# Optimization experiments

Hardware: AMD Instinct MI355X
Metric: run time of the kernel (lower is better)

Reference implementation:

```python
import jax, jax.numpy as jnp
import numpy as np

NUM_LEVELS = 8
BASE_RES = 16
MAX_RES = 1024
TABLE_SIZE = 2 ** 17
FEAT = 2
ALPHA_SHIFT = 5.0
ALPHA_SCALE = 1.0

_growth = np.exp((np.log(MAX_RES) - np.log(BASE_RES)) / (NUM_LEVELS - 1))
SCALINGS = np.floor(BASE_RES * _growth ** np.arange(NUM_LEVELS)).astype(np.float32)  # per-level grid res
CORNERS = np.array([[(i >> 2) & 1, (i >> 1) & 1, i & 1] for i in range(8)], dtype=np.int32)  # voxel corners
PRIMES = np.array([1, 2654435761, 805459861], dtype=np.uint32)  # nerfstudio hash primes


def hash_encode(pos, table):
    # pos: [N,3] in [0,1]; table: [NUM_LEVELS*TABLE_SIZE, FEAT]
    scaled = pos[:, None, :] * jnp.asarray(SCALINGS)[None, :, None]              # [N,L,3]
    f = jnp.floor(scaled)
    w = scaled - f                                                               # trilinear weights
    idx = f.astype(jnp.int32)[:, :, None, :] + jnp.asarray(CORNERS)[None, None]  # [N,L,8,3]
    h = idx.astype(jnp.uint32) * jnp.asarray(PRIMES)
    hashed = (h[..., 0] ^ h[..., 1] ^ h[..., 2]) % TABLE_SIZE                    # [N,L,8]
    hashed = hashed.astype(jnp.int32) + (jnp.arange(NUM_LEVELS, dtype=jnp.int32) * TABLE_SIZE)[None, :, None]
    feats = table[hashed]                                                        # [N,L,8,F] gather
    cw = jnp.where(jnp.asarray(CORNERS)[None, None] == 1, w[:, :, None, :], 1.0 - w[:, :, None, :]).prod(-1)
    out = (feats * cw[..., None]).sum(2)                                         # [N,L,F]
    return out.reshape(pos.shape[0], NUM_LEVELS * FEAT)


def setup_inputs():
    key = jax.random.key(0)
    ks = jax.random.split(key, 8)
    R, S = 8192, 48
    return {
        "positions": jax.random.normal(ks[0], (R, S, 3), jnp.float32),
        "c2ws": jax.random.normal(ks[1], (R, 3, 4), jnp.float32) * 0.5,
        "aabb": jnp.array([[-1.0, -1.0, -1.0], [1.0, 1.0, 1.0]], jnp.float32),
        "table": jax.random.uniform(ks[2], (NUM_LEVELS * TABLE_SIZE, FEAT), jnp.float32, -1e-4, 1e-4),
        "w1": jax.random.normal(ks[3], (16, 32), jnp.float32) * 0.25,
        "b1": jnp.zeros((32,), jnp.float32),
        "w2": jax.random.normal(ks[4], (32, 16), jnp.float32) * 0.18,
        "b2": jnp.zeros((16,), jnp.float32),
        "hw1": jax.random.normal(ks[5], (16, 64), jnp.float32) * 0.25,
        "hb1": jnp.zeros((64,), jnp.float32),
        "hw2": jax.random.normal(ks[6], (64, 1), jnp.float32) * 0.125,
        "hb2": jnp.zeros((1,), jnp.float32),
    }


def reference(positions, c2ws, aabb, table, w1, b1, w2, b2, hw1, hb1, hw2, hb2):
    R, S = positions.shape[:2]
    rot = c2ws[:, :3, :3]
    trans = c2ws[:, :3, 3]
    rot_t = jnp.swapaxes(rot, 1, 2)                          # w2c rotation = R^T
    t_w2c = -jnp.einsum('rij,rj->ri', rot_t, trans)          # w2c translation = -R^T t
    pos = jnp.einsum('rij,rsj->rsi', rot_t, positions) + t_w2c[:, None, :]
    pos = (pos - aabb[0]) / (aabb[1] - aabb[0])              # SceneBox.get_normalized_positions
    selector = jnp.all((pos > 0.0) & (pos < 1.0), axis=-1)   # inside unit cube
    pos = pos * selector[..., None]
    enc = hash_encode(pos.reshape(-1, 3), table)             # [N, 16]
    h = jax.nn.relu(enc @ w1 + b1) @ w2 + b2                 # mlp_base -> geo features
    o = jax.nn.relu(h @ hw1 + hb1) @ hw2 + hb2               # mlp_head -> alpha logits
    o = o.reshape(R, S, -1)
    return ALPHA_SCALE * jax.nn.sigmoid(o - ALPHA_SHIFT) * selector[..., None]
```

## Files before the change

kernel.cpp:

```cpp
#include <hip/hip_runtime.h>
#include <math.h>
#include <stdint.h>

#define NLEV 8
#define TSIZE 131072
#define TMASK (TSIZE - 1)

__global__ __launch_bounds__(256, 4) void rif_kernel(
    const float* __restrict__ positions,
    const float* __restrict__ c2ws,
    const float* __restrict__ aabb,
    const float* __restrict__ table,
    const float* __restrict__ w1, const float* __restrict__ b1,
    const float* __restrict__ w2, const float* __restrict__ b2,
    const float* __restrict__ hw1, const float* __restrict__ hb1,
    const float* __restrict__ hw2, const float* __restrict__ hb2,
    float* __restrict__ out, int total, int S)
{
    __shared__ float sw1[512];
    __shared__ float sb1[32];
    __shared__ float sw2[512];
    __shared__ float sb2[16];
    __shared__ float shw1[1024];
    __shared__ float shb1[64];
    __shared__ float shw2[64];
    __shared__ float shb2[1];

    for (int i = threadIdx.x; i < 512; i += 256) { sw1[i] = w1[i]; sw2[i] = w2[i]; }
    for (int i = threadIdx.x; i < 1024; i += 256) shw1[i] = hw1[i];
    if (threadIdx.x < 64) { shb1[threadIdx.x] = hb1[threadIdx.x]; shw2[threadIdx.x] = hw2[threadIdx.x]; }
    if (threadIdx.x < 32) sb1[threadIdx.x] = b1[threadIdx.x];
    if (threadIdx.x < 16) sb2[threadIdx.x] = b2[threadIdx.x];
    if (threadIdx.x == 0) shb2[0] = hb2[0];
    __syncthreads();

    int gid = blockIdx.x * blockDim.x + threadIdx.x;
    if (gid >= total) return;
    int r = gid / S;

    const float* p = positions + (size_t)gid * 3;
    const float* c = c2ws + (size_t)r * 12;
    float px = p[0], py = p[1], pz = p[2];
    float c00 = c[0], c01 = c[1], c02 = c[2],  t0 = c[3];
    float c10 = c[4], c11 = c[5], c12 = c[6],  t1 = c[7];
    float c20 = c[8], c21 = c[9], c22 = c[10], t2 = c[11];

    float m0 = __fadd_rn(__fadd_rn(__fmul_rn(c00, px), __fmul_rn(c10, py)), __fmul_rn(c20, pz));
    float m1 = __fadd_rn(__fadd_rn(__fmul_rn(c01, px), __fmul_rn(c11, py)), __fmul_rn(c21, pz));
    float m2 = __fadd_rn(__fadd_rn(__fmul_rn(c02, px), __fmul_rn(c12, py)), __fmul_rn(c22, pz));
    float n0 = __fadd_rn(__fadd_rn(__fmul_rn(c00, t0), __fmul_rn(c10, t1)), __fmul_rn(c20, t2));
    float n1 = __fadd_rn(__fadd_rn(__fmul_rn(c01, t0), __fmul_rn(c11, t1)), __fmul_rn(c21, t2));
    float n2 = __fadd_rn(__fadd_rn(__fmul_rn(c02, t0), __fmul_rn(c12, t1)), __fmul_rn(c22, t2));
    float posx = __fsub_rn(m0, n0);
    float posy = __fsub_rn(m1, n1);
    float posz = __fsub_rn(m2, n2);

    float a0x = aabb[0], a0y = aabb[1], a0z = aabb[2];
    float a1x = aabb[3], a1y = aabb[4], a1z = aabb[5];
    posx = __fdiv_rn(__fsub_rn(posx, a0x), __fsub_rn(a1x, a0x));
    posy = __fdiv_rn(__fsub_rn(posy, a0y), __fsub_rn(a1y, a0y));
    posz = __fdiv_rn(__fsub_rn(posz, a0z), __fsub_rn(a1z, a0z));

    bool sel = (posx > 0.f) & (posx < 1.f) & (posy > 0.f) & (posy < 1.f) & (posz > 0.f) & (posz < 1.f);
    if (!sel) { out[gid] = 0.f; return; }

    const float kScale[8] = {16.f, 28.f, 52.f, 95.f, 172.f, 312.f, 565.f, 1024.f};

    float wxs[8], wys[8], wzs[8];
    float2 ft[8][8];
    #pragma unroll
    for (int l = 0; l < NLEV; ++l) {
        float sc = kScale[l];
        float sx = posx * sc, sy = posy * sc, sz = posz * sc;
        float fx = floorf(sx), fy = floorf(sy), fz = floorf(sz);
        wxs[l] = sx - fx; wys[l] = sy - fy; wzs[l] = sz - fz;
        uint32_t ix = (uint32_t)(int)fx, iy = (uint32_t)(int)fy, iz = (uint32_t)(int)fz;
        uint32_t hy0 = iy * 2654435761u, hy1 = hy0 + 2654435761u;
        uint32_t hz0 = iz * 805459861u,  hz1 = hz0 + 805459861u;
        const float2* tab = (const float2*)table + (size_t)l * TSIZE;
        #pragma unroll
        for (int cc = 0; cc < 8; ++cc) {
            uint32_t cx = (cc >> 2) & 1, cy = (cc >> 1) & 1, cz = cc & 1;
            uint32_t hh = ((ix + cx) ^ (cy ? hy1 : hy0) ^ (cz ? hz1 : hz0)) & TMASK;
            ft[l][cc] = tab[hh];
        }
    }

    float enc[16];
    #pragma unroll
    for (int l = 0; l < NLEV; ++l) {
        float wx = wxs[l], wy = wys[l], wz = wzs[l];
        float ux = 1.f - wx, uy = 1.f - wy, uz = 1.f - wz;
        float q00 = uy * uz, q01 = uy * wz, q10 = wy * uz, q11 = wy * wz;
        float f0, f1;
        f0 = ft[l][0].x * (ux * q00); f1 = ft[l][0].y * (ux * q00);
        f0 = fmaf(ft[l][1].x, ux * q01, f0); f1 = fmaf(ft[l][1].y, ux * q01, f1);
        f0 = fmaf(ft[l][2].x, ux * q10, f0); f1 = fmaf(ft[l][2].y, ux * q10, f1);
        f0 = fmaf(ft[l][3].x, ux * q11, f0); f1 = fmaf(ft[l][3].y, ux * q11, f1);
        f0 = fmaf(ft[l][4].x, wx * q00, f0); f1 = fmaf(ft[l][4].y, wx * q00, f1);
        f0 = fmaf(ft[l][5].x, wx * q01, f0); f1 = fmaf(ft[l][5].y, wx * q01, f1);
        f0 = fmaf(ft[l][6].x, wx * q10, f0); f1 = fmaf(ft[l][6].y, wx * q10, f1);
        f0 = fmaf(ft[l][7].x, wx * q11, f0); f1 = fmaf(ft[l][7].y, wx * q11, f1);
        enc[2 * l] = f0;
        enc[2 * l + 1] = f1;
    }

    float h1[32];
    #pragma unroll
    for (int j = 0; j < 32; ++j) h1[j] = sb1[j];
    #pragma unroll
    for (int i = 0; i < 16; ++i) {
        float e = enc[i];
        #pragma unroll
        for (int j = 0; j < 32; ++j) h1[j] = fmaf(e, sw1[i * 32 + j], h1[j]);
    }
    #pragma unroll
    for (int j = 0; j < 32; ++j) h1[j] = fmaxf(h1[j], 0.f);

    float h2[16];
    #pragma unroll
    for (int j = 0; j < 16; ++j) h2[j] = sb2[j];
    #pragma unroll
    for (int i = 0; i < 32; ++i) {
        float e = h1[i];
        #pragma unroll
        for (int j = 0; j < 16; ++j) h2[j] = fmaf(e, sw2[i * 16 + j], h2[j]);
    }

    float o = shb2[0];
    #pragma unroll
    for (int j = 0; j < 64; ++j) {
        float acc = shb1[j];
        #pragma unroll
        for (int i = 0; i < 16; ++i) acc = fmaf(h2[i], shw1[i * 64 + j], acc);
        o = fmaf(fmaxf(acc, 0.f), shw2[j], o);
    }

    float x = o - 5.0f;
    out[gid] = 1.0f / (1.0f + expf(-x));
}

extern "C" void kernel_launch(void* const* d_in, const int* in_sizes, int n_in,
                              void* d_out, int out_size, void* d_ws, size_t ws_size,
                              hipStream_t stream) {
    const float* positions = (const float*)d_in[0];
    const float* c2ws      = (const float*)d_in[1];
    const float* aabb      = (const float*)d_in[2];
    const float* table     = (const float*)d_in[3];
    const float* w1  = (const float*)d_in[4];
    const float* b1  = (const float*)d_in[5];
    const float* w2  = (const float*)d_in[6];
    const float* b2  = (const float*)d_in[7];
    const float* hw1 = (const float*)d_in[8];
    const float* hb1 = (const float*)d_in[9];
    const float* hw2 = (const float*)d_in[10];
    const float* hb2 = (const float*)d_in[11];

    int R = in_sizes[1] / 12;
    int total = in_sizes[0] / 3;
    int S = total / R;

    int threads = 256;
    int blocks = (total + threads - 1) / threads;
    hipLaunchKernelGGL(rif_kernel, dim3(blocks), dim3(threads), 0, stream,
                       positions, c2ws, aabb, table,
                       w1, b1, w2, b2, hw1, hb1, hw2, hb2,
                       (float*)d_out, total, S);
}
```

Before: 69.09 us.

## Compact in-box samples via atomic index list before hash encoding and MLP

Measured after the change: 140.0 us. +102.6%, slower.

```diff
diff --git a/kernel.cpp b/kernel.cpp
--- a/kernel.cpp
+++ b/kernel.cpp
@@ -6,7 +6,95 @@
 #define TSIZE 131072
 #define TMASK (TSIZE - 1)
 
-__global__ __launch_bounds__(256, 4) void rif_kernel(
+__device__ __forceinline__ void transform_pos(
+    const float* __restrict__ positions, const float* __restrict__ c2ws,
+    const float* __restrict__ aabb, int gid, int S,
+    float& posx, float& posy, float& posz, bool& sel)
+{
+    int r = gid / S;
+    const float* p = positions + (size_t)gid * 3;
+    const float* c = c2ws + (size_t)r * 12;
+    float px = p[0], py = p[1], pz = p[2];
+    float c00 = c[0], c01 = c[1], c02 = c[2],  t0 = c[3];
+    float c10 = c[4], c11 = c[5], c12 = c[6],  t1 = c[7];
+    float c20 = c[8], c21 = c[9], c22 = c[10], t2 = c[11];
+
+    float m0 = __fadd_rn(__fadd_rn(__fmul_rn(c00, px), __fmul_rn(c10, py)), __fmul_rn(c20, pz));
+    float m1 = __fadd_rn(__fadd_rn(__fmul_rn(c01, px), __fmul_rn(c11, py)), __fmul_rn(c21, pz));
+    float m2 = __fadd_rn(__fadd_rn(__fmul_rn(c02, px), __fmul_rn(c12, py)), __fmul_rn(c22, pz));
+    float n0 = __fadd_rn(__fadd_rn(__fmul_rn(c00, t0), __fmul_rn(c10, t1)), __fmul_rn(c20, t2));
+    float n1 = __fadd_rn(__fadd_rn(__fmul_rn(c01, t0), __fmul_rn(c11, t1)), __fmul_rn(c21, t2));
+    float n2 = __fadd_rn(__fadd_rn(__fmul_rn(c02, t0), __fmul_rn(c12, t1)), __fmul_rn(c22, t2));
+    float x0 = __fsub_rn(m0, n0);
+    float x1 = __fsub_rn(m1, n1);
+    float x2 = __fsub_rn(m2, n2);
+
+    float a0x = aabb[0], a0y = aabb[1], a0z = aabb[2];
+    float a1x = aabb[3], a1y = aabb[4], a1z = aabb[5];
+    posx = __fdiv_rn(__fsub_rn(x0, a0x), __fsub_rn(a1x, a0x));
+    posy = __fdiv_rn(__fsub_rn(x1, a0y), __fsub_rn(a1y, a0y));
+    posz = __fdiv_rn(__fsub_rn(x2, a0z), __fsub_rn(a1z, a0z));
+    sel = (posx > 0.f) & (posx < 1.f) & (posy > 0.f) & (posy < 1.f) & (posz > 0.f) & (posz < 1.f);
+}
+
+__device__ __forceinline__ float mlp_and_sigmoid(
+    const float* enc,
+    const float* sw1, const float* sb1, const float* sw2, const float* sb2,
+    const float* shw1, const float* shb1, const float* shw2, const float* shb2)
+{
+    float h1[32];
+    #pragma unroll
+    for (int j = 0; j < 32; ++j) h1[j] = sb1[j];
+    #pragma unroll
+    for (int i = 0; i < 16; ++i) {
+        float e = enc[i];
+        #pragma unroll
+        for (int j = 0; j < 32; ++j) h1[j] = fmaf(e, sw1[i * 32 + j], h1[j]);
+    }
+    #pragma unroll
+    for (int j = 0; j < 32; ++j) h1[j] = fmaxf(h1[j], 0.f);
+
+    float h2[16];
+    #pragma unroll
+    for (int j = 0; j < 16; ++j) h2[j] = sb2[j];
+    #pragma unroll
+    for (int i = 0; i < 32; ++i) {
+        float e = h1[i];
+        #pragma unroll
+        for (int j = 0; j < 16; ++j) h2[j] = fmaf(e, sw2[i * 16 + j], h2[j]);
+    }
+
+    float o = shb2[0];
+    #pragma unroll
+    for (int j = 0; j < 64; ++j) {
+        float acc = shb1[j];
+        #pragma unroll
+        for (int i = 0; i < 16; ++i) acc = fmaf(h2[i], shw1[i * 64 + j], acc);
+        o = fmaf(fmaxf(acc, 0.f), shw2[j], o);
+    }
+    float x = o - 5.0f;
+    return 1.0f / (1.0f + expf(-x));
+}
+
+__global__ __launch_bounds__(256) void rif_select(
+    const float* __restrict__ positions,
+    const float* __restrict__ c2ws,
+    const float* __restrict__ aabb,
+    float* __restrict__ out,
+    uint32_t* __restrict__ cnt,
+    uint32_t* __restrict__ idxbuf,
+    int total, int S)
+{
+    int gid = blockIdx.x * blockDim.x + threadIdx.x;
+    if (gid >= total) return;
+    float posx, posy, posz; bool sel;
+    transform_pos(positions, c2ws, aabb, gid, S, posx, posy, posz, sel);
+    if (!sel) { out[gid] = 0.f; return; }
+    uint32_t slot = atomicAdd(cnt, 1u);
+    idxbuf[slot] = (uint32_t)gid;
+}
+
+__global__ __launch_bounds__(256, 2) void rif_main(
     const float* __restrict__ positions,
     const float* __restrict__ c2ws,
     const float* __restrict__ aabb,
@@ -15,7 +103,10 @@
     const float* __restrict__ w2, const float* __restrict__ b2,
     const float* __restrict__ hw1, const float* __restrict__ hb1,
     const float* __restrict__ hw2, const float* __restrict__ hb2,
-    float* __restrict__ out, int total, int S)
+    float* __restrict__ out,
+    const uint32_t* __restrict__ cnt,
+    const uint32_t* __restrict__ idxbuf,
+    int total, int S)
 {
     __shared__ float sw1[512];
     __shared__ float sb1[32];
@@ -34,35 +125,13 @@
     if (threadIdx.x == 0) shb2[0] = hb2[0];
     __syncthreads();
 
-    int gid = blockIdx.x * blockDim.x + threadIdx.x;
-    if (gid >= total) return;
-    int r = gid / S;
-
-    const float* p = positions + (size_t)gid * 3;
-    const float* c = c2ws + (size_t)r * 12;
-    float px = p[0], py = p[1], pz = p[2];
-    float c00 = c[0], c01 = c[1], c02 = c[2],  t0 = c[3];
-    float c10 = c[4], c11 = c[5], c12 = c[6],  t1 = c[7];
-    float c20 = c[8], c21 = c[9], c22 = c[10], t2 = c[11];
-
-    float m0 = __fadd_rn(__fadd_rn(__fmul_rn(c00, px), __fmul_rn(c10, py)), __fmul_rn(c20, pz));
-    float m1 = __fadd_rn(__fadd_rn(__fmul_rn(c01, px), __fmul_rn(c11, py)), __fmul_rn(c21, pz));
-    float m2 = __fadd_rn(__fadd_rn(__fmul_rn(c02, px), __fmul_rn(c12, py)), __fmul_rn(c22, pz));
-    float n0 = __fadd_rn(__fadd_rn(__fmul_rn(c00, t0), __fmul_rn(c10, t1)), __fmul_rn(c20, t2));
-    float n1 = __fadd_rn(__fadd_rn(__fmul_rn(c01, t0), __fmul_rn(c11, t1)), __fmul_rn(c21, t2));
-    float n2 = __fadd_rn(__fadd_rn(__fmul_rn(c02, t0), __fmul_rn(c12, t1)), __fmul_rn(c22, t2));
-    float posx = __fsub_rn(m0, n0);
-    float posy = __fsub_rn(m1, n1);
-    float posz = __fsub_rn(m2, n2);
-
-    float a0x = aabb[0], a0y = aabb[1], a0z = aabb[2];
-    float a1x = aabb[3], a1y = aabb[4], a1z = aabb[5];
-    posx = __fdiv_rn(__fsub_rn(posx, a0x), __fsub_rn(a1x, a0x));
-    posy = __fdiv_rn(__fsub_rn(posy, a0y), __fsub_rn(a1y, a0y));
-    posz = __fdiv_rn(__fsub_rn(posz, a0z), __fsub_rn(a1z, a0z));
-
-    bool sel = (posx > 0.f) & (posx < 1.f) & (posy > 0.f) & (posy < 1.f) & (posz > 0.f) & (posz < 1.f);
-    if (!sel) { out[gid] = 0.f; return; }
+    uint32_t count = *cnt;
+    uint32_t i = blockIdx.x * blockDim.x + threadIdx.x;
+    if (i >= count) return;
+    int gid = (int)idxbuf[i];
+
+    float posx, posy, posz; bool sel;
+    transform_pos(positions, c2ws, aabb, gid, S, posx, posy, posz, sel);
 
     const float kScale[8] = {16.f, 28.f, 52.f, 95.f, 172.f, 312.f, 565.f, 1024.f};
 
@@ -85,6 +154,7 @@
             ft[l][cc] = tab[hh];
         }
     }
+    __builtin_amdgcn_sched_barrier(0);
 
     float enc[16];
     #pragma unroll
@@ -105,39 +175,69 @@
         enc[2 * l + 1] = f1;
     }
 
-    float h1[32];
-    #pragma unroll
-    for (int j = 0; j < 32; ++j) h1[j] = sb1[j];
-    #pragma unroll
-    for (int i = 0; i < 16; ++i) {
-        float e = enc[i];
-        #pragma unroll
-        for (int j = 0; j < 32; ++j) h1[j] = fmaf(e, sw1[i * 32 + j], h1[j]);
-    }
-    #pragma unroll
-    for (int j = 0; j < 32; ++j) h1[j] = fmaxf(h1[j], 0.f);
-
-    float h2[16];
-    #pragma unroll
-    for (int j = 0; j < 16; ++j) h2[j] = sb2[j];
-    #pragma unroll
-    for (int i = 0; i < 32; ++i) {
-        float e = h1[i];
-        #pragma unroll
-        for (int j = 0; j < 16; ++j) h2[j] = fmaf(e, sw2[i * 16 + j], h2[j]);
-    }
-
-    float o = shb2[0];
-    #pragma unroll
-    for (int j = 0; j < 64; ++j) {
-        float acc = shb1[j];
-        #pragma unroll
-        for (int i = 0; i < 16; ++i) acc = fmaf(h2[i], shw1[i * 64 + j], acc);
-        o = fmaf(fmaxf(acc, 0.f), shw2[j], o);
-    }
-
-    float x = o - 5.0f;
-    out[gid] = 1.0f / (1.0f + expf(-x));
+    out[gid] = mlp_and_sigmoid(enc, sw1, sb1, sw2, sb2, shw1, shb1, shw2, shb2);
+}
+
+__global__ __launch_bounds__(256, 4) void rif_mono(
+    const float* __restrict__ positions,
+    const float* __restrict__ c2ws,
+    const float* __restrict__ aabb,
+    const float* __restrict__ table,
+    const float* __restrict__ w1, const float* __restrict__ b1,
+    const float* __restrict__ w2, const float* __restrict__ b2,
+    const float* __restrict__ hw1, const float* __restrict__ hb1,
+    const float* __restrict__ hw2, const float* __restrict__ hb2,
+    float* __restrict__ out, int total, int S)
+{
+    __shared__ float sw1[512];
+    __shared__ float sb1[32];
+    __shared__ float sw2[512];
+    __shared__ float sb2[16];
+    __shared__ float shw1[1024];
+    __shared__ float shb1[64];
+    __shared__ float shw2[64];
+    __shared__ float shb2[1];
+
+    for (int i = threadIdx.x; i < 512; i += 256) { sw1[i] = w1[i]; sw2[i] = w2[i]; }
+    for (int i = threadIdx.x; i < 1024; i += 256) shw1[i] = hw1[i];
+    if (threadIdx.x < 64) { shb1[threadIdx.x] = hb1[threadIdx.x]; shw2[threadIdx.x] = hw2[threadIdx.x]; }
+    if (threadIdx.x < 32) sb1[threadIdx.x] = b1[threadIdx.x];
+    if (threadIdx.x < 16) sb2[threadIdx.x] = b2[threadIdx.x];
+    if (threadIdx.x == 0) shb2[0] = hb2[0];
+    __syncthreads();
+
+    int gid = blockIdx.x * blockDim.x + threadIdx.x;
+    if (gid >= total) return;
+    float posx, posy, posz; bool sel;
+    transform_pos(positions, c2ws, aabb, gid, S, posx, posy, posz, sel);
+    if (!sel) { out[gid] = 0.f; return; }
+
+    const float kScale[8] = {16.f, 28.f, 52.f, 95.f, 172.f, 312.f, 565.f, 1024.f};
+    float enc[16];
+    #pragma unroll
+    for (int l = 0; l < NLEV; ++l) {
+        float sc = kScale[l];
+        float sx = posx * sc, sy = posy * sc, sz = posz * sc;
+        float fx = floorf(sx), fy = floorf(sy), fz = floorf(sz);
+        float wx = sx - fx, wy = sy - fy, wz = sz - fz;
+        uint32_t ix = (uint32_t)(int)fx, iy = (uint32_t)(int)fy, iz = (uint32_t)(int)fz;
+        uint32_t hy0 = iy * 2654435761u, hy1 = hy0 + 2654435761u;
+        uint32_t hz0 = iz * 805459861u,  hz1 = hz0 + 805459861u;
+        const float2* tab = (const float2*)table + (size_t)l * TSIZE;
+        float f0 = 0.f, f1 = 0.f;
+        #pragma unroll
+        for (int cc = 0; cc < 8; ++cc) {
+            uint32_t cx = (cc >> 2) & 1, cy = (cc >> 1) & 1, cz = cc & 1;
+            uint32_t hh = ((ix + cx) ^ (cy ? hy1 : hy0) ^ (cz ? hz1 : hz0)) & TMASK;
+            float wgt = (cx ? wx : 1.f - wx) * (cy ? wy : 1.f - wy) * (cz ? wz : 1.f - wz);
+            float2 ftv = tab[hh];
+            f0 = fmaf(ftv.x, wgt, f0);
+            f1 = fmaf(ftv.y, wgt, f1);
+        }
+        enc[2 * l] = f0;
+        enc[2 * l + 1] = f1;
+    }
+    out[gid] = mlp_and_sigmoid(enc, sw1, sb1, sw2, sb2, shw1, shb1, shw2, shb2);
 }
 
 extern "C" void kernel_launch(void* const* d_in, const int* in_sizes, int n_in,
@@ -162,8 +262,22 @@
 
     int threads = 256;
     int blocks = (total + threads - 1) / threads;
-    hipLaunchKernelGGL(rif_kernel, dim3(blocks), dim3(threads), 0, stream,
-                       positions, c2ws, aabb, table,
-                       w1, b1, w2, b2, hw1, hb1, hw2, hb2,
-                       (float*)d_out, total, S);
-}
+
+    size_t needed = 64 + (size_t)total * 4;
+    if (ws_size >= needed) {
+        uint32_t* cnt = (uint32_t*)d_ws;
+        uint32_t* idxbuf = (uint32_t*)((char*)d_ws + 64);
+        hipMemsetAsync(d_ws, 0, 4, stream);
+        hipLaunchKernelGGL(rif_select, dim3(blocks), dim3(threads), 0, stream,
+                           positions, c2ws, aabb, (float*)d_out, cnt, idxbuf, total, S);
+        hipLaunchKernelGGL(rif_main, dim3(blocks), dim3(threads), 0, stream,
+                           positions, c2ws, aabb, table,
+                           w1, b1, w2, b2, hw1, hb1, hw2, hb2,
+                           (float*)d_out, cnt, idxbuf, total, S);
+    } else {
+        hipLaunchKernelGGL(rif_mono, dim3(blocks), dim3(threads), 0, stream,
+                           positions, c2ws, aabb, table,
+                           w1, b1, w2, b2, hw1, hb1, hw2, hb2,
+                           (float*)d_out, total, S);
+    }
+}
```
